# Optimization experiments

Measured on AMD Instinct MI355X. Metric: run time of the kernel, lower is better.

Reference implementation:

```python
import jax, jax.numpy as jnp
import numpy as np

B, F, INP, S = 2048, 50, 2, 1024
LN_EPS = 1e-3
UPDATE_BIAS = -1.0
_TRUNC = 0.8796256610342398  # trunc-normal std correction from weight_init


def _std(fan_in, fan_out):
    return np.sqrt(2.0 / (fan_in + fan_out)) / _TRUNC


def setup_inputs() -> dict:
    key = jax.random.key(0)
    k_act, k_emb, k_gru, k_dec = jax.random.split(key, 4)
    return {
        "action": jax.random.normal(k_act, (B, F, INP), dtype=jnp.float32),
        "W_emb": jax.random.normal(k_emb, (INP, S), dtype=jnp.float32) * _std(INP, S),
        "W_gru": jax.random.normal(k_gru, (2 * S, 3 * S), dtype=jnp.float32) * _std(2 * S, 3 * S),
        "ln_gamma": jnp.ones((3 * S,), dtype=jnp.float32),
        "ln_beta": jnp.zeros((3 * S,), dtype=jnp.float32),
        "W_dec": jax.random.normal(k_dec, (S, INP), dtype=jnp.float32) * _std(S, INP),
        "b_dec": jnp.zeros((INP,), dtype=jnp.float32),
    }


def reference(action, W_emb, W_gru, ln_gamma, ln_beta, W_dec, b_dec):
    # action: [b, f, inp]
    emb = jnp.einsum("bfi,is->bfs", action, W_emb)  # [b, f, s]

    def step(prev, x_t):
        # prev, x_t: [b, s]
        parts = jnp.concatenate([x_t, prev], axis=-1) @ W_gru  # [b, 3s]
        mu = parts.mean(-1, keepdims=True)
        var = parts.var(-1, keepdims=True)
        parts = (parts - mu) / jnp.sqrt(var + LN_EPS) * ln_gamma + ln_beta
        reset, cand, update = jnp.split(parts, 3, axis=-1)
        reset = jax.nn.sigmoid(reset)
        cand = jnp.tanh(reset * cand)
        update = jax.nn.sigmoid(update + UPDATE_BIAS)
        h = update * cand + (1.0 - update) * prev
        return h, None

    prev0 = jnp.zeros_like(emb[:, 0])
    h_last, _ = jax.lax.scan(step, prev0, jnp.swapaxes(emb, 0, 1))  # scan over f
    outputs = h_last @ W_dec + b_dec  # [b, inp]
    return h_last[:, None], outputs[:, None]
```

## Files before the change

kernel.cpp:

```cpp
#include <hip/hip_runtime.h>

typedef unsigned short u16;
typedef unsigned int   u32;
typedef _Float16       f16;

#define B_SZ 2048
#define S_SZ 1024
#define N3   3072
#define F_SZ 50

typedef f16    f16x8 __attribute__((ext_vector_type(8)));
typedef f16    f16x4 __attribute__((ext_vector_type(4)));
typedef float  f32x4 __attribute__((ext_vector_type(4)));
typedef u32    u32x4 __attribute__((ext_vector_type(4)));

__device__ __forceinline__ void glds16(const void* g, void* l) {
    __builtin_amdgcn_global_load_lds(
        (const __attribute__((address_space(1))) u32*)g,
        (__attribute__((address_space(3))) u32*)l, 16, 0, 0);
}

__global__ __launch_bounds__(256) void make_mx(
    const float* __restrict__ We, const float* __restrict__ Wg,
    float* __restrict__ Mx)
{
    int j  = blockIdx.x * 256 + threadIdx.x;
    int k0 = blockIdx.y * 64;
    float s0 = 0.f, s1 = 0.f;
    #pragma unroll 4
    for (int k = k0; k < k0 + 64; k++) {
        float w = Wg[(size_t)k * N3 + j];
        s0 += We[k] * w;
        s1 += We[S_SZ + k] * w;
    }
    atomicAdd(&Mx[j], s0);
    atomicAdd(&Mx[N3 + j], s1);
}

__global__ __launch_bounds__(256) void transpose_w(
    const float* __restrict__ Wg, f16* __restrict__ Wt)
{
    __shared__ float tile[32][33];
    int n0 = blockIdx.x * 32, k0 = blockIdx.y * 32;
    int c = threadIdx.x & 31, r = threadIdx.x >> 5;
    #pragma unroll
    for (int s = 0; s < 4; s++) {
        int rr = r + s * 8;
        tile[rr][c] = Wg[(size_t)(S_SZ + k0 + rr) * N3 + n0 + c];
    }
    __syncthreads();
    #pragma unroll
    for (int s = 0; s < 4; s++) {
        int rr = r + s * 8;
        Wt[(size_t)(n0 + rr) * S_SZ + k0 + c] = (f16)tile[c][rr];
    }
}

__global__ __launch_bounds__(256) void gemm_step(
    const f16* __restrict__ Wt,
    const f16* __restrict__ hh,
    const float* __restrict__ Mx,
    const float* __restrict__ act,
    f16* __restrict__ parts,
    int t)
{
    __shared__ __align__(16) f16 As[64 * 64];
    __shared__ __align__(16) f16 Bs[128 * 64];

    const int bid = blockIdx.x;
    const int xcd = bid & 7;
    const int loc = bid >> 3;
    const int mt  = (xcd >> 2) * 16 + (loc & 15);
    const int nt  = (xcd & 3) * 6 + (loc >> 4);
    const int m0 = mt * 64;
    const int n0 = nt * 128;

    const int tid  = threadIdx.x;
    const int lane = tid & 63;
    const int wave = tid >> 6;
    const int wr = (wave >> 1) * 32;
    const int wc = (wave & 1) * 64;
    const int quad = lane >> 4, lrow = lane & 15;
    const int swz = (lrow & 7) * 8;

    const int lrow8 = lane >> 3;
    const int scolh = ((lane & 7) * 8) ^ (lrow8 * 8);

    f32x4 acc[2][4];
    #pragma unroll
    for (int i = 0; i < 2; i++)
        #pragma unroll
        for (int j = 0; j < 4; j++)
            acc[i][j] = (f32x4){0.f, 0.f, 0.f, 0.f};

    for (int kb = 0; kb < S_SZ; kb += 64) {
        __syncthreads();
        #pragma unroll
        for (int c = 0; c < 2; c++) {
            int ch = wave * 2 + c;
            int row = ch * 8 + lrow8;
            glds16(&hh[(size_t)(m0 + row) * S_SZ + kb + scolh], &As[ch * 512]);
        }
        #pragma unroll
        for (int c = 0; c < 4; c++) {
            int ch = wave * 4 + c;
            int row = ch * 8 + lrow8;
            glds16(&Wt[(size_t)(n0 + row) * S_SZ + kb + scolh], &Bs[ch * 512]);
        }
        __syncthreads();
        #pragma unroll
        for (int kk = 0; kk < 64; kk += 32) {
            f16x8 a[2], b[4];
            #pragma unroll
            for (int i = 0; i < 2; i++)
                a[i] = __builtin_bit_cast(f16x8,
                    *(const u32x4*)&As[(wr + i * 16 + lrow) * 64 +
                                       ((kk + quad * 8) ^ swz)]);
            #pragma unroll
            for (int j = 0; j < 4; j++)
                b[j] = __builtin_bit_cast(f16x8,
                    *(const u32x4*)&Bs[(wc + j * 16 + lrow) * 64 +
                                       ((kk + quad * 8) ^ swz)]);
            #pragma unroll
            for (int i = 0; i < 2; i++)
                #pragma unroll
                for (int j = 0; j < 4; j++)
                    acc[i][j] = __builtin_amdgcn_mfma_f32_16x16x32_f16(
                        a[i], b[j], acc[i][j], 0, 0, 0);
        }
    }

    #pragma unroll
    for (int i = 0; i < 2; i++) {
        #pragma unroll
        for (int rr = 0; rr < 4; rr++) {
            int m = m0 + wr + i * 16 + quad * 4 + rr;
            float a0 = act[((size_t)m * F_SZ + t) * 2 + 0];
            float a1 = act[((size_t)m * F_SZ + t) * 2 + 1];
            #pragma unroll
            for (int j = 0; j < 4; j++) {
                int n = n0 + wc + j * 16 + lrow;
                parts[(size_t)m * N3 + n] =
                    (f16)(acc[i][j][rr] + a0 * Mx[n] + a1 * Mx[N3 + n]);
            }
        }
    }
}

__global__ __launch_bounds__(256) void ln_gate_step(
    const f16* __restrict__ parts,
    const float* __restrict__ gamma,
    const float* __restrict__ beta,
    f16* __restrict__ hh,
    float* __restrict__ hout,
    int t)
{
    const int tid = threadIdx.x;
    const int r2  = tid >> 7;
    const int tl  = tid & 127;
    const int row = blockIdx.x * 2 + r2;
    const f16* p = parts + (size_t)row * N3 + tl * 8;

    float v[24];
    float s = 0.f, ss = 0.f;
    #pragma unroll
    for (int g = 0; g < 3; g++) {
        f16x8 x = *(const f16x8*)(p + g * S_SZ);
        #pragma unroll
        for (int e = 0; e < 8; e++) {
            float f = (float)x[e];
            v[g * 8 + e] = f;
            s += f; ss += f * f;
        }
    }
    #pragma unroll
    for (int o = 1; o < 64; o <<= 1) {
        s  += __shfl_xor(s, o);
        ss += __shfl_xor(ss, o);
    }
    __shared__ float red[8];
    int wave = tid >> 6, lane = tid & 63;
    if (lane == 0) { red[wave] = s; red[4 + wave] = ss; }
    __syncthreads();
    float S  = red[r2 * 2] + red[r2 * 2 + 1];
    float SS = red[4 + r2 * 2] + red[4 + r2 * 2 + 1];
    float mean = S * (1.f / N3);
    float var  = SS * (1.f / N3) - mean * mean;
    float rstd = rsqrtf(var + 1e-3f);

    float nv[24];
    #pragma unroll
    for (int g = 0; g < 3; g++) {
        f32x4 g0 = *(const f32x4*)(gamma + g * S_SZ + tl * 8);
        f32x4 g1 = *(const f32x4*)(gamma + g * S_SZ + tl * 8 + 4);
        f32x4 b0 = *(const f32x4*)(beta  + g * S_SZ + tl * 8);
        f32x4 b1 = *(const f32x4*)(beta  + g * S_SZ + tl * 8 + 4);
        #pragma unroll
        for (int e = 0; e < 4; e++) {
            nv[g * 8 + e]     = (v[g * 8 + e]     - mean) * rstd * g0[e] + b0[e];
            nv[g * 8 + e + 4] = (v[g * 8 + e + 4] - mean) * rstd * g1[e] + b1[e];
        }
    }

    size_t hbase = (size_t)row * S_SZ + tl * 8;
    f16x8 hp = *(const f16x8*)(hh + hbase);
    f16x8 hs;
    f32x4 ho0, ho1;
    #pragma unroll
    for (int e = 0; e < 8; e++) {
        float rg = 1.f / (1.f + __expf(-nv[e]));
        float x  = rg * nv[8 + e];
        float tt = __expf(-2.f * fabsf(x));
        float cg = __builtin_copysignf((1.f - tt) / (1.f + tt), x);
        float ug = 1.f / (1.f + __expf(-(nv[16 + e] - 1.f)));
        float hv = ug * cg + (1.f - ug) * (float)hp[e];
        hs[e] = (f16)hv;
        if (e < 4) ho0[e] = hv; else ho1[e - 4] = hv;
    }
    *(f16x8*)(hh + hbase) = hs;
    if (t == F_SZ - 1) {
        *(f32x4*)(hout + hbase)     = ho0;
        *(f32x4*)(hout + hbase + 4) = ho1;
    }
}

__global__ __launch_bounds__(256) void final_out(
    const float* __restrict__ h, const float* __restrict__ Wd,
    const float* __restrict__ bd, float* __restrict__ out)
{
    int row = blockIdx.x * 4 + (threadIdx.x >> 6);
    int lane = threadIdx.x & 63;
    const float* hr = h + (size_t)row * S_SZ;
    float s0 = 0.f, s1 = 0.f;
    #pragma unroll
    for (int k = lane; k < S_SZ; k += 64) {
        float x = hr[k];
        s0 += x * Wd[k * 2];
        s1 += x * Wd[k * 2 + 1];
    }
    #pragma unroll
    for (int o = 32; o > 0; o >>= 1) {
        s0 += __shfl_down(s0, o);
        s1 += __shfl_down(s1, o);
    }
    if (lane == 0) {
        out[(size_t)B_SZ * S_SZ + row * 2 + 0] = s0 + bd[0];
        out[(size_t)B_SZ * S_SZ + row * 2 + 1] = s1 + bd[1];
    }
}

extern "C" void kernel_launch(void* const* d_in, const int* in_sizes, int n_in,
                              void* d_out, int out_size, void* d_ws, size_t ws_size,
                              hipStream_t stream)
{
    const float* act = (const float*)d_in[0];
    const float* We  = (const float*)d_in[1];
    const float* Wg  = (const float*)d_in[2];
    const float* lng = (const float*)d_in[3];
    const float* lnb = (const float*)d_in[4];
    const float* Wd  = (const float*)d_in[5];
    const float* bd  = (const float*)d_in[6];
    float* out = (float*)d_out;

    char* ws = (char*)d_ws;
    f16*   Wt    = (f16*)ws;
    float* Mx    = (float*)(ws + 6291456);
    f16*   hh    = (f16*)(ws + 6316032);
    f16*   parts = (f16*)(ws + 10510336);

    hipMemsetAsync(hh, 0, (size_t)B_SZ * S_SZ * 2, stream);
    hipMemsetAsync(Mx, 0, 2 * N3 * 4, stream);
    make_mx<<<dim3(N3 / 256, 16), 256, 0, stream>>>(We, Wg, Mx);
    transpose_w<<<dim3(N3 / 32, S_SZ / 32), 256, 0, stream>>>(Wg, Wt);

    for (int t = 0; t < F_SZ; t++) {
        gemm_step<<<dim3(768), 256, 0, stream>>>(Wt, hh, Mx, act, parts, t);
        ln_gate_step<<<B_SZ / 2, 256, 0, stream>>>(parts, lng, lnb, hh, out, t);
    }
    final_out<<<B_SZ / 4, 256, 0, stream>>>(out, Wd, bd, out);
}
```

Baseline: 1.482 ms.

## Fuse GEMM and LayerNorm-gate step via per-row-tile atomic counters

```diff
diff --git a/kernel.cpp b/kernel.cpp
--- a/kernel.cpp
+++ b/kernel.cpp
@@ -10,7 +10,6 @@
 #define F_SZ 50
 
 typedef f16    f16x8 __attribute__((ext_vector_type(8)));
-typedef f16    f16x4 __attribute__((ext_vector_type(4)));
 typedef float  f32x4 __attribute__((ext_vector_type(4)));
 typedef u32    u32x4 __attribute__((ext_vector_type(4)));
 
@@ -56,22 +55,27 @@
     }
 }
 
-__global__ __launch_bounds__(256) void gemm_step(
+__global__ __launch_bounds__(256, 3) void gemm_ln_step(
     const f16* __restrict__ Wt,
-    const f16* __restrict__ hh,
+    f16* __restrict__ hh,
     const float* __restrict__ Mx,
     const float* __restrict__ act,
     f16* __restrict__ parts,
+    const float* __restrict__ gamma,
+    const float* __restrict__ beta,
+    float* __restrict__ hout,
+    u32* __restrict__ cnt,
     int t)
 {
     __shared__ __align__(16) f16 As[64 * 64];
     __shared__ __align__(16) f16 Bs[128 * 64];
+    __shared__ float red[8];
 
     const int bid = blockIdx.x;
     const int xcd = bid & 7;
     const int loc = bid >> 3;
-    const int mt  = (xcd >> 2) * 16 + (loc & 15);
-    const int nt  = (xcd & 3) * 6 + (loc >> 4);
+    const int mt  = (loc & 3) * 8 + xcd;
+    const int nt  = loc >> 2;
     const int m0 = mt * 64;
     const int n0 = nt * 128;
 
@@ -145,82 +149,86 @@
             }
         }
     }
-}
-
-__global__ __launch_bounds__(256) void ln_gate_step(
-    const f16* __restrict__ parts,
-    const float* __restrict__ gamma,
-    const float* __restrict__ beta,
-    f16* __restrict__ hh,
-    float* __restrict__ hout,
-    int t)
-{
-    const int tid = threadIdx.x;
-    const int r2  = tid >> 7;
-    const int tl  = tid & 127;
-    const int row = blockIdx.x * 2 + r2;
-    const f16* p = parts + (size_t)row * N3 + tl * 8;
-
-    float v[24];
-    float s = 0.f, ss = 0.f;
-    #pragma unroll
-    for (int g = 0; g < 3; g++) {
-        f16x8 x = *(const f16x8*)(p + g * S_SZ);
+
+    __syncthreads();
+    u32* c = cnt + t * 32 + mt;
+    if (tid == 0) atomicAdd(c, 1u);
+    if (nt >= 16) return;
+
+    if (tid == 0) {
+        while (__hip_atomic_load(c, __ATOMIC_RELAXED,
+                                 __HIP_MEMORY_SCOPE_AGENT) < 24u)
+            __builtin_amdgcn_s_sleep(8);
+    }
+    __syncthreads();
+    __threadfence();
+
+    const int r2 = tid >> 7;
+    const int tl = tid & 127;
+    for (int rp = 0; rp < 2; ++rp) {
+        const int row = m0 + nt * 4 + rp * 2 + r2;
+        const f16* p = parts + (size_t)row * N3 + tl * 8;
+
+        float v[24];
+        float s = 0.f, ss = 0.f;
+        #pragma unroll
+        for (int g = 0; g < 3; g++) {
+            f16x8 x = *(const f16x8*)(p + g * S_SZ);
+            #pragma unroll
+            for (int e = 0; e < 8; e++) {
+                float f = (float)x[e];
+                v[g * 8 + e] = f;
+                s += f; ss += f * f;
+            }
+        }
+        #pragma unroll
+        for (int o = 1; o < 64; o <<= 1) {
+            s  += __shfl_xor(s, o);
+            ss += __shfl_xor(ss, o);
+        }
+        if (lane == 0) { red[wave] = s; red[4 + wave] = ss; }
+        __syncthreads();
+        float S  = red[r2 * 2] + red[r2 * 2 + 1];
+        float SS = red[4 + r2 * 2] + red[4 + r2 * 2 + 1];
+        __syncthreads();
+        float mean = S * (1.f / N3);
+        float var  = SS * (1.f / N3) - mean * mean;
+        float rstd = rsqrtf(var + 1e-3f);
+
+        float nv[24];
+        #pragma unroll
+        for (int g = 0; g < 3; g++) {
+            f32x4 g0 = *(const f32x4*)(gamma + g * S_SZ + tl * 8);
+            f32x4 g1 = *(const f32x4*)(gamma + g * S_SZ + tl * 8 + 4);
+            f32x4 b0 = *(const f32x4*)(beta  + g * S_SZ + tl * 8);
+            f32x4 b1 = *(const f32x4*)(beta  + g * S_SZ + tl * 8 + 4);
+            #pragma unroll
+            for (int e = 0; e < 4; e++) {
+                nv[g * 8 + e]     = (v[g * 8 + e]     - mean) * rstd * g0[e] + b0[e];
+                nv[g * 8 + e + 4] = (v[g * 8 + e + 4] - mean) * rstd * g1[e] + b1[e];
+            }
+        }
+
+        size_t hbase = (size_t)row * S_SZ + tl * 8;
+        f16x8 hp = *(const f16x8*)(hh + hbase);
+        f16x8 hs;
+        f32x4 ho0, ho1;
         #pragma unroll
         for (int e = 0; e < 8; e++) {
-            float f = (float)x[e];
-            v[g * 8 + e] = f;
-            s += f; ss += f * f;
-        }
-    }
-    #pragma unroll
-    for (int o = 1; o < 64; o <<= 1) {
-        s  += __shfl_xor(s, o);
-        ss += __shfl_xor(ss, o);
-    }
-    __shared__ float red[8];
-    int wave = tid >> 6, lane = tid & 63;
-    if (lane == 0) { red[wave] = s; red[4 + wave] = ss; }
-    __syncthreads();
-    float S  = red[r2 * 2] + red[r2 * 2 + 1];
-    float SS = red[4 + r2 * 2] + red[4 + r2 * 2 + 1];
-    float mean = S * (1.f / N3);
-    float var  = SS * (1.f / N3) - mean * mean;
-    float rstd = rsqrtf(var + 1e-3f);
-
-    float nv[24];
-    #pragma unroll
-    for (int g = 0; g < 3; g++) {
-        f32x4 g0 = *(const f32x4*)(gamma + g * S_SZ + tl * 8);
-        f32x4 g1 = *(const f32x4*)(gamma + g * S_SZ + tl * 8 + 4);
-        f32x4 b0 = *(const f32x4*)(beta  + g * S_SZ + tl * 8);
-        f32x4 b1 = *(const f32x4*)(beta  + g * S_SZ + tl * 8 + 4);
-        #pragma unroll
-        for (int e = 0; e < 4; e++) {
-            nv[g * 8 + e]     = (v[g * 8 + e]     - mean) * rstd * g0[e] + b0[e];
-            nv[g * 8 + e + 4] = (v[g * 8 + e + 4] - mean) * rstd * g1[e] + b1[e];
-        }
-    }
-
-    size_t hbase = (size_t)row * S_SZ + tl * 8;
-    f16x8 hp = *(const f16x8*)(hh + hbase);
-    f16x8 hs;
-    f32x4 ho0, ho1;
-    #pragma unroll
-    for (int e = 0; e < 8; e++) {
-        float rg = 1.f / (1.f + __expf(-nv[e]));
-        float x  = rg * nv[8 + e];
-        float tt = __expf(-2.f * fabsf(x));
-        float cg = __builtin_copysignf((1.f - tt) / (1.f + tt), x);
-        float ug = 1.f / (1.f + __expf(-(nv[16 + e] - 1.f)));
-        float hv = ug * cg + (1.f - ug) * (float)hp[e];
-        hs[e] = (f16)hv;
-        if (e < 4) ho0[e] = hv; else ho1[e - 4] = hv;
-    }
-    *(f16x8*)(hh + hbase) = hs;
-    if (t == F_SZ - 1) {
-        *(f32x4*)(hout + hbase)     = ho0;
-        *(f32x4*)(hout + hbase + 4) = ho1;
+            float rg = 1.f / (1.f + __expf(-nv[e]));
+            float x  = rg * nv[8 + e];
+            float tt = __expf(-2.f * fabsf(x));
+            float cg = __builtin_copysignf((1.f - tt) / (1.f + tt), x);
+            float ug = 1.f / (1.f + __expf(-(nv[16 + e] - 1.f)));
+            float hv = ug * cg + (1.f - ug) * (float)hp[e];
+            hs[e] = (f16)hv;
+            if (e < 4) ho0[e] = hv; else ho1[e - 4] = hv;
+        }
+        *(f16x8*)(hh + hbase) = hs;
+        if (t == F_SZ - 1) {
+            *(f32x4*)(hout + hbase)     = ho0;
+            *(f32x4*)(hout + hbase + 4) = ho1;
+        }
     }
 }
 
@@ -267,15 +275,17 @@
     float* Mx    = (float*)(ws + 6291456);
     f16*   hh    = (f16*)(ws + 6316032);
     f16*   parts = (f16*)(ws + 10510336);
+    u32*   cnt   = (u32*)(ws + 23093248);
 
     hipMemsetAsync(hh, 0, (size_t)B_SZ * S_SZ * 2, stream);
     hipMemsetAsync(Mx, 0, 2 * N3 * 4, stream);
+    hipMemsetAsync(cnt, 0, F_SZ * 32 * 4, stream);
     make_mx<<<dim3(N3 / 256, 16), 256, 0, stream>>>(We, Wg, Mx);
     transpose_w<<<dim3(N3 / 32, S_SZ / 32), 256, 0, stream>>>(Wg, Wt);
 
     for (int t = 0; t < F_SZ; t++) {
-        gemm_step<<<dim3(768), 256, 0, stream>>>(Wt, hh, Mx, act, parts, t);
-        ln_gate_step<<<B_SZ / 2, 256, 0, stream>>>(parts, lng, lnb, hh, out, t);
+        gemm_ln_step<<<dim3(768), 256, 0, stream>>>(
+            Wt, hh, Mx, act, parts, lng, lnb, out, cnt, t);
     }
     final_out<<<B_SZ / 4, 256, 0, stream>>>(out, Wd, bd, out);
 }
```

New measurement: 4.850 ms. +227.3%, slower.

## Skip first-step GEMM, use one wave per row in gate kernel, fuse decoder

Applied to the files above, without the earlier changes.

```diff
diff --git a/kernel.cpp b/kernel.cpp
--- a/kernel.cpp
+++ b/kernel.cpp
@@ -10,7 +10,6 @@
 #define F_SZ 50
 
 typedef f16    f16x8 __attribute__((ext_vector_type(8)));
-typedef f16    f16x4 __attribute__((ext_vector_type(4)));
 typedef float  f32x4 __attribute__((ext_vector_type(4)));
 typedef u32    u32x4 __attribute__((ext_vector_type(4)));
 
@@ -152,100 +151,119 @@
     const float* __restrict__ gamma,
     const float* __restrict__ beta,
     f16* __restrict__ hh,
-    float* __restrict__ hout,
+    float* __restrict__ out,
+    const float* __restrict__ act,
+    const float* __restrict__ Mx,
+    const float* __restrict__ Wd,
+    const float* __restrict__ bd,
     int t)
 {
-    const int tid = threadIdx.x;
-    const int r2  = tid >> 7;
-    const int tl  = tid & 127;
-    const int row = blockIdx.x * 2 + r2;
-    const f16* p = parts + (size_t)row * N3 + tl * 8;
-
-    float v[24];
+    const int lane = threadIdx.x & 63;
+    const int row  = blockIdx.x * 4 + (threadIdx.x >> 6);
+    const int u0   = lane * 16;
+
+    float v[48];
     float s = 0.f, ss = 0.f;
-    #pragma unroll
-    for (int g = 0; g < 3; g++) {
-        f16x8 x = *(const f16x8*)(p + g * S_SZ);
-        #pragma unroll
-        for (int e = 0; e < 8; e++) {
-            float f = (float)x[e];
-            v[g * 8 + e] = f;
-            s += f; ss += f * f;
-        }
-    }
+    if (t == 0) {
+        const float a0 = act[(size_t)row * F_SZ * 2 + 0];
+        const float a1 = act[(size_t)row * F_SZ * 2 + 1];
+        #pragma unroll
+        for (int g = 0; g < 3; g++) {
+            #pragma unroll
+            for (int e = 0; e < 16; e += 4) {
+                f32x4 m0 = *(const f32x4*)(Mx + g * S_SZ + u0 + e);
+                f32x4 m1 = *(const f32x4*)(Mx + N3 + g * S_SZ + u0 + e);
+                #pragma unroll
+                for (int q = 0; q < 4; q++) {
+                    float f = a0 * m0[q] + a1 * m1[q];
+                    v[g * 16 + e + q] = f;
+                    s += f; ss += f * f;
+                }
+            }
+        }
+    } else {
+        const f16* p = parts + (size_t)row * N3 + u0;
+        #pragma unroll
+        for (int g = 0; g < 3; g++) {
+            f16x8 x0 = *(const f16x8*)(p + g * S_SZ);
+            f16x8 x1 = *(const f16x8*)(p + g * S_SZ + 8);
+            #pragma unroll
+            for (int e = 0; e < 8; e++) {
+                float f0 = (float)x0[e], f1 = (float)x1[e];
+                v[g * 16 + e]     = f0;
+                v[g * 16 + 8 + e] = f1;
+                s += f0 + f1; ss += f0 * f0 + f1 * f1;
+            }
+        }
+    }
+
     #pragma unroll
     for (int o = 1; o < 64; o <<= 1) {
         s  += __shfl_xor(s, o);
         ss += __shfl_xor(ss, o);
     }
-    __shared__ float red[8];
-    int wave = tid >> 6, lane = tid & 63;
-    if (lane == 0) { red[wave] = s; red[4 + wave] = ss; }
-    __syncthreads();
-    float S  = red[r2 * 2] + red[r2 * 2 + 1];
-    float SS = red[4 + r2 * 2] + red[4 + r2 * 2 + 1];
-    float mean = S * (1.f / N3);
-    float var  = SS * (1.f / N3) - mean * mean;
-    float rstd = rsqrtf(var + 1e-3f);
-
-    float nv[24];
+    const float mean = s * (1.f / N3);
+    const float var  = ss * (1.f / N3) - mean * mean;
+    const float rstd = rsqrtf(var + 1e-3f);
+
     #pragma unroll
     for (int g = 0; g < 3; g++) {
-        f32x4 g0 = *(const f32x4*)(gamma + g * S_SZ + tl * 8);
-        f32x4 g1 = *(const f32x4*)(gamma + g * S_SZ + tl * 8 + 4);
-        f32x4 b0 = *(const f32x4*)(beta  + g * S_SZ + tl * 8);
-        f32x4 b1 = *(const f32x4*)(beta  + g * S_SZ + tl * 8 + 4);
-        #pragma unroll
-        for (int e = 0; e < 4; e++) {
-            nv[g * 8 + e]     = (v[g * 8 + e]     - mean) * rstd * g0[e] + b0[e];
-            nv[g * 8 + e + 4] = (v[g * 8 + e + 4] - mean) * rstd * g1[e] + b1[e];
-        }
-    }
-
-    size_t hbase = (size_t)row * S_SZ + tl * 8;
-    f16x8 hp = *(const f16x8*)(hh + hbase);
-    f16x8 hs;
-    f32x4 ho0, ho1;
-    #pragma unroll
-    for (int e = 0; e < 8; e++) {
-        float rg = 1.f / (1.f + __expf(-nv[e]));
-        float x  = rg * nv[8 + e];
+        #pragma unroll
+        for (int e = 0; e < 16; e += 4) {
+            f32x4 gm = *(const f32x4*)(gamma + g * S_SZ + u0 + e);
+            f32x4 bt = *(const f32x4*)(beta  + g * S_SZ + u0 + e);
+            #pragma unroll
+            for (int q = 0; q < 4; q++)
+                v[g * 16 + e + q] =
+                    (v[g * 16 + e + q] - mean) * rstd * gm[q] + bt[q];
+        }
+    }
+
+    const size_t hbase = (size_t)row * S_SZ + u0;
+    f16x8 hp0 = {}, hp1 = {};
+    if (t > 0) {
+        hp0 = *(const f16x8*)(hh + hbase);
+        hp1 = *(const f16x8*)(hh + hbase + 8);
+    }
+    f16x8 hs0, hs1;
+    float hv[16];
+    #pragma unroll
+    for (int e = 0; e < 16; e++) {
+        float rg = 1.f / (1.f + __expf(-v[e]));
+        float x  = rg * v[16 + e];
         float tt = __expf(-2.f * fabsf(x));
         float cg = __builtin_copysignf((1.f - tt) / (1.f + tt), x);
-        float ug = 1.f / (1.f + __expf(-(nv[16 + e] - 1.f)));
-        float hv = ug * cg + (1.f - ug) * (float)hp[e];
-        hs[e] = (f16)hv;
-        if (e < 4) ho0[e] = hv; else ho1[e - 4] = hv;
-    }
-    *(f16x8*)(hh + hbase) = hs;
+        float ug = 1.f / (1.f + __expf(-(v[32 + e] - 1.f)));
+        float hpv = (e < 8) ? (float)hp0[e] : (float)hp1[e - 8];
+        float h = ug * cg + (1.f - ug) * hpv;
+        hv[e] = h;
+        if (e < 8) hs0[e] = (f16)h; else hs1[e - 8] = (f16)h;
+    }
+    *(f16x8*)(hh + hbase)     = hs0;
+    *(f16x8*)(hh + hbase + 8) = hs1;
+
     if (t == F_SZ - 1) {
-        *(f32x4*)(hout + hbase)     = ho0;
-        *(f32x4*)(hout + hbase + 4) = ho1;
-    }
-}
-
-__global__ __launch_bounds__(256) void final_out(
-    const float* __restrict__ h, const float* __restrict__ Wd,
-    const float* __restrict__ bd, float* __restrict__ out)
-{
-    int row = blockIdx.x * 4 + (threadIdx.x >> 6);
-    int lane = threadIdx.x & 63;
-    const float* hr = h + (size_t)row * S_SZ;
-    float s0 = 0.f, s1 = 0.f;
-    #pragma unroll
-    for (int k = lane; k < S_SZ; k += 64) {
-        float x = hr[k];
-        s0 += x * Wd[k * 2];
-        s1 += x * Wd[k * 2 + 1];
-    }
-    #pragma unroll
-    for (int o = 32; o > 0; o >>= 1) {
-        s0 += __shfl_down(s0, o);
-        s1 += __shfl_down(s1, o);
-    }
-    if (lane == 0) {
-        out[(size_t)B_SZ * S_SZ + row * 2 + 0] = s0 + bd[0];
-        out[(size_t)B_SZ * S_SZ + row * 2 + 1] = s1 + bd[1];
+        #pragma unroll
+        for (int e = 0; e < 16; e += 4) {
+            f32x4 o4 = { hv[e], hv[e + 1], hv[e + 2], hv[e + 3] };
+            *(f32x4*)(out + hbase + e) = o4;
+        }
+        float s0 = 0.f, s1 = 0.f;
+        #pragma unroll
+        for (int e = 0; e < 16; e++) {
+            const float2 w = *(const float2*)(Wd + (size_t)(u0 + e) * 2);
+            s0 += hv[e] * w.x;
+            s1 += hv[e] * w.y;
+        }
+        #pragma unroll
+        for (int o = 32; o > 0; o >>= 1) {
+            s0 += __shfl_down(s0, o);
+            s1 += __shfl_down(s1, o);
+        }
+        if (lane == 0) {
+            out[(size_t)B_SZ * S_SZ + row * 2 + 0] = s0 + bd[0];
+            out[(size_t)B_SZ * S_SZ + row * 2 + 1] = s1 + bd[1];
+        }
     }
 }
 
@@ -268,14 +286,16 @@
     f16*   hh    = (f16*)(ws + 6316032);
     f16*   parts = (f16*)(ws + 10510336);
 
-    hipMemsetAsync(hh, 0, (size_t)B_SZ * S_SZ * 2, stream);
     hipMemsetAsync(Mx, 0, 2 * N3 * 4, stream);
     make_mx<<<dim3(N3 / 256, 16), 256, 0, stream>>>(We, Wg, Mx);
     transpose_w<<<dim3(N3 / 32, S_SZ / 32), 256, 0, stream>>>(Wg, Wt);
 
-    for (int t = 0; t < F_SZ; t++) {
+    ln_gate_step<<<B_SZ / 4, 256, 0, stream>>>(
+        parts, lng, lnb, hh, out, act, Mx, Wd, bd, 0);
+
+    for (int t = 1; t < F_SZ; t++) {
         gemm_step<<<dim3(768), 256, 0, stream>>>(Wt, hh, Mx, act, parts, t);
-        ln_gate_step<<<B_SZ / 2, 256, 0, stream>>>(parts, lng, lnb, hh, out, t);
-    }
-    final_out<<<B_SZ / 4, 256, 0, stream>>>(out, Wd, bd, out);
-}
+        ln_gate_step<<<B_SZ / 4, 256, 0, stream>>>(
+            parts, lng, lnb, hh, out, act, Mx, Wd, bd, t);
+    }
+}
```

After: 1.569 ms. +5.9%, slower.
